# Optimization experiments

Measured on AMD Instinct MI355X. Metric: run time of the kernel, lower is better.

## Reference

```python
import jax, jax.numpy as jnp
import numpy as np
import math

DIM = 512
HEADS = 8
DHEAD = DIM // HEADS            # 64
NB_FEATURES = int(DHEAD * math.log(DHEAD))  # 266
B, N = 2, 2048
CHUNK = 128                     # chunk size for the causal scan
EPS = 1e-4


def gaussian_orthogonal_random_matrix(nb_rows, nb_cols, rng):
    # blocks of orthogonal rows (Q^T of QR of a gaussian), scaled by chi-distributed norms
    blocks = []
    n_full = nb_rows // nb_cols
    for _ in range(n_full):
        q, _ = np.linalg.qr(rng.standard_normal((nb_cols, nb_cols)))
        blocks.append(q.T)
    rem = nb_rows - n_full * nb_cols
    if rem > 0:
        q, _ = np.linalg.qr(rng.standard_normal((nb_cols, nb_cols)))
        blocks.append(q.T[:rem])
    mat = np.concatenate(blocks, axis=0)
    multiplier = np.linalg.norm(rng.standard_normal((nb_rows, nb_cols)), axis=1)
    return (multiplier[:, None] * mat).astype(np.float32)


def setup_inputs() -> dict:
    key = jax.random.key(0)
    k1, k2, k3 = jax.random.split(key, 3)
    rng = np.random.default_rng(0)
    x = jax.random.normal(k1, (B, N, DIM), dtype=jnp.float32)
    w_qkv = jax.random.normal(k2, (DIM, 3 * DIM), dtype=jnp.float32) / math.sqrt(DIM)
    w_out = jax.random.normal(k3, (DIM, DIM), dtype=jnp.float32) / math.sqrt(DIM)
    b_out = jnp.zeros((DIM,), dtype=jnp.float32)
    proj = jnp.asarray(gaussian_orthogonal_random_matrix(NB_FEATURES, DHEAD, rng))
    return {"x": x, "w_qkv": w_qkv, "w_out": w_out, "b_out": b_out, "proj": proj}


def softmax_kernel(data, proj, is_query):
    # data: [b,h,n,d], proj: [m,d]
    d = data.shape[-1]
    data_normalizer = d ** -0.25
    ratio = proj.shape[0] ** -0.5
    data_dash = jnp.einsum('bhnd,md->bhnm', data_normalizer * data, proj)
    diag_data = jnp.sum(data * data, axis=-1, keepdims=True) * 0.5 * (data_normalizer ** 2)
    if is_query:
        stab = jnp.max(data_dash, axis=-1, keepdims=True)
    else:
        stab = jnp.max(data_dash)
    return ratio * (jnp.exp(data_dash - diag_data - stab) + EPS)


def causal_linear_attention(q, k, v, chunk=CHUNK):
    # q,k: [b,h,n,m]; v: [b,h,n,d]
    # out_n = sum_m q_nm * (sum_{i<=n} k_im v_i) / (sum_{i<=n} k_im)   (per-feature normalization,
    # identical to causal_linear_attention_noncuda), computed in chunks for memory efficiency.
    b, h, n, m = q.shape
    d = v.shape[-1]
    nc = n // chunk
    qc = jnp.moveaxis(q.reshape(b, h, nc, chunk, m), 2, 0)  # [nc,b,h,C,m]
    kc = jnp.moveaxis(k.reshape(b, h, nc, chunk, m), 2, 0)
    vc = jnp.moveaxis(v.reshape(b, h, nc, chunk, d), 2, 0)

    def step(carry, inp):
        kv_state, ksum_state = carry            # [b,h,m,d], [b,h,m]
        qch, kch, vch = inp                     # [b,h,C,m], [b,h,C,m], [b,h,C,d]
        ksum = ksum_state[:, :, None, :] + jnp.cumsum(kch, axis=2)          # [b,h,C,m]
        ctx = kv_state[:, :, None, :, :] + jnp.cumsum(
            jnp.einsum('bhcm,bhcd->bhcmd', kch, vch), axis=2)               # [b,h,C,m,d]
        out = jnp.einsum('bhcm,bhcmd->bhcd', qch, ctx / ksum[..., None])
        return (ctx[:, :, -1], ksum[:, :, -1]), out

    init = (jnp.zeros((b, h, m, d), q.dtype), jnp.zeros((b, h, m), q.dtype))
    _, outs = jax.lax.scan(step, init, (qc, kc, vc))
    return jnp.moveaxis(outs, 0, 2).reshape(b, h, n, d)


def reference(x, w_qkv, w_out, b_out, proj):
    b, n, _ = x.shape
    qkv = x @ w_qkv                                   # [b,n,3*dim]
    q, k, v = jnp.split(qkv, 3, axis=-1)
    split = lambda t: t.reshape(b, n, HEADS, DHEAD).transpose(0, 2, 1, 3)  # b h n d
    q, k, v = split(q), split(k), split(v)
    qp = softmax_kernel(q, proj, is_query=True)       # [b,h,n,m]
    kp = softmax_kernel(k, proj, is_query=False)
    out = causal_linear_attention(qp, kp, v)          # [b,h,n,d]
    out = out.transpose(0, 2, 1, 3).reshape(b, n, DIM)
    return out @ w_out + b_out
```

## Files before the change

kernel.cpp:

```cpp
#include <hip/hip_runtime.h>
#include <math.h>

#define DIMX 512
#define NHEADS 8
#define DH 64
#define MF 266
#define MP 272
#define MPS 288
#define NB 2
#define NSEQ 2048
#define NROWS (NB*NSEQ)
#define NBH 16
#define CHK 64
#define NCH 32
#define EPSF 1e-4f
#define LDT 40
#define LDP 72

typedef __attribute__((ext_vector_type(8))) short short8;
typedef __attribute__((ext_vector_type(4))) float f32x4;
typedef unsigned short ushort_t;

__device__ __forceinline__ unsigned fkey(float f){
    unsigned u = __float_as_uint(f);
    return (f < 0.0f) ? ~u : (u | 0x80000000u);
}
__device__ __forceinline__ float fdec(unsigned k){
    unsigned u = (k & 0x80000000u) ? (k & 0x7fffffffu) : ~k;
    return __uint_as_float(u);
}
__device__ __forceinline__ float b2f(ushort_t u){
    return __uint_as_float(((unsigned)u) << 16);
}

__device__ __forceinline__ void bsplit(float a, ushort_t& h, ushort_t& l){
    unsigned u = __float_as_uint(a);
    unsigned r = (u + 0x7fffu + ((u >> 16) & 1u)) & 0xffff0000u;
    h = (ushort_t)(r >> 16);
    float res = a - __uint_as_float(r);
    unsigned v = __float_as_uint(res);
    unsigned r2 = v + 0x7fffu + ((v >> 16) & 1u);
    l = (ushort_t)(r2 >> 16);
}

__global__ __launch_bounds__(256) void split_kernel(
    const float* __restrict__ A, ushort_t* __restrict__ H, ushort_t* __restrict__ L, int total4)
{
    int i = blockIdx.x * 256 + threadIdx.x;
    if (i >= total4) return;
    float4 f = ((const float4*)A)[i];
    ushort_t h0,h1,h2,h3,l0,l1,l2,l3;
    bsplit(f.x,h0,l0); bsplit(f.y,h1,l1); bsplit(f.z,h2,l2); bsplit(f.w,h3,l3);
    ((ushort4*)H)[i] = make_ushort4(h0,h1,h2,h3);
    ((ushort4*)L)[i] = make_ushort4(l0,l1,l2,l3);
}

__global__ __launch_bounds__(256) void splitT_kernel(
    const float* __restrict__ W, ushort_t* __restrict__ Th, ushort_t* __restrict__ Tl,
    int K, int N)
{
    __shared__ ushort_t Sh[64][72], Sl[64][72];
    const int k0 = blockIdx.y * 64, n0 = blockIdx.x * 64;
    const int tid = threadIdx.x;
    {
        const int kk = tid >> 4, nq = (tid & 15) * 4;
        for (int p = 0; p < 4; p++) {
            int k = p*16 + kk;
            float4 f = *(const float4*)&W[(size_t)(k0 + k)*N + n0 + nq];
            ushort_t h, l;
            bsplit(f.x,h,l); Sh[nq+0][k]=h; Sl[nq+0][k]=l;
            bsplit(f.y,h,l); Sh[nq+1][k]=h; Sl[nq+1][k]=l;
            bsplit(f.z,h,l); Sh[nq+2][k]=h; Sl[nq+2][k]=l;
            bsplit(f.w,h,l); Sh[nq+3][k]=h; Sl[nq+3][k]=l;
        }
    }
    __syncthreads();
    {
        const int n = tid >> 2, ks = (tid & 3) * 16;
        for (int q = 0; q < 2; q++) {
            uint4 vh = *(const uint4*)&Sh[n][ks + q*8];
            uint4 vl = *(const uint4*)&Sl[n][ks + q*8];
            *(uint4*)&Th[(size_t)(n0 + n)*K + k0 + ks + q*8] = vh;
            *(uint4*)&Tl[(size_t)(n0 + n)*K + k0 + ks + q*8] = vl;
        }
    }
}

__global__ __launch_bounds__(256) void splitP_kernel(
    const float* __restrict__ proj, ushort_t* __restrict__ ph, ushort_t* __restrict__ pl,
    unsigned* __restrict__ gmax, float nrm)
{
    int idx = blockIdx.x * 256 + threadIdx.x;
    if (idx == 0) *gmax = 0u;
    if (idx >= MPS*64/4) return;
    int m = idx >> 4, kq = (idx & 15) * 4;
    ushort4 h4 = make_ushort4(0,0,0,0), l4 = make_ushort4(0,0,0,0);
    if (m < MF) {
        float4 f = *(const float4*)&proj[m*64 + kq];
        ushort_t hh[4], ll[4];
        bsplit(f.x*nrm,hh[0],ll[0]); bsplit(f.y*nrm,hh[1],ll[1]);
        bsplit(f.z*nrm,hh[2],ll[2]); bsplit(f.w*nrm,hh[3],ll[3]);
        h4 = make_ushort4(hh[0],hh[1],hh[2],hh[3]);
        l4 = make_ushort4(ll[0],ll[1],ll[2],ll[3]);
    }
    *(ushort4*)&ph[(size_t)m*64 + kq] = h4;
    *(ushort4*)&pl[(size_t)m*64 + kq] = l4;
}

__global__ __launch_bounds__(256) void gemm_bf16s(
    const ushort_t* __restrict__ Ah, const ushort_t* __restrict__ Al,
    const ushort_t* __restrict__ Bh, const ushort_t* __restrict__ Bl,
    const float* __restrict__ bias, float* __restrict__ C,
    int M, int N, int K)
{
    __shared__ ushort_t sAh[128*LDT], sAl[128*LDT], sBh[128*LDT], sBl[128*LDT];
    const int tid = threadIdx.x;
    const int m0 = blockIdx.y * 128, n0 = blockIdx.x * 128;
    const int lane = tid & 63, w = tid >> 6;
    const int wr = w >> 1, wc = w & 1;
    const int lr = lane & 15;
    const int lsu = (lane >> 4) * 8;
    const int r = tid >> 1, sg = (tid & 1) * 16;
    const size_t gA = (size_t)(m0 + r)*K + sg;
    const size_t gB = (size_t)(n0 + r)*K + sg;

    f32x4 acc[4][4];
    #pragma unroll
    for (int i=0;i<4;i++)
        #pragma unroll
        for (int j=0;j<4;j++) acc[i][j] = (f32x4){0.f,0.f,0.f,0.f};

    for (int k0 = 0; k0 < K; k0 += 32) {
        uint4 a0 = *(const uint4*)&Ah[gA + k0];
        uint4 a1 = *(const uint4*)&Ah[gA + k0 + 8];
        uint4 a2 = *(const uint4*)&Al[gA + k0];
        uint4 a3 = *(const uint4*)&Al[gA + k0 + 8];
        uint4 b0 = *(const uint4*)&Bh[gB + k0];
        uint4 b1 = *(const uint4*)&Bh[gB + k0 + 8];
        uint4 b2 = *(const uint4*)&Bl[gB + k0];
        uint4 b3 = *(const uint4*)&Bl[gB + k0 + 8];
        __syncthreads();
        *(uint4*)&sAh[r*LDT + sg]     = a0;
        *(uint4*)&sAh[r*LDT + sg + 8] = a1;
        *(uint4*)&sAl[r*LDT + sg]     = a2;
        *(uint4*)&sAl[r*LDT + sg + 8] = a3;
        *(uint4*)&sBh[r*LDT + sg]     = b0;
        *(uint4*)&sBh[r*LDT + sg + 8] = b1;
        *(uint4*)&sBl[r*LDT + sg]     = b2;
        *(uint4*)&sBl[r*LDT + sg + 8] = b3;
        __syncthreads();
        short8 afh[4], afl[4], bfh[4], bfl[4];
        #pragma unroll
        for (int f = 0; f < 4; f++) {
            int ra = (wr*64 + f*16 + lr)*LDT + lsu;
            int rb = (wc*64 + f*16 + lr)*LDT + lsu;
            afh[f] = *(const short8*)&sAh[ra];
            afl[f] = *(const short8*)&sAl[ra];
            bfh[f] = *(const short8*)&sBh[rb];
            bfl[f] = *(const short8*)&sBl[rb];
        }
        #pragma unroll
        for (int i = 0; i < 4; i++)
            #pragma unroll
            for (int j = 0; j < 4; j++) {
                acc[i][j] = __builtin_amdgcn_mfma_f32_16x16x32_bf16(afh[i], bfh[j], acc[i][j], 0, 0, 0);
                acc[i][j] = __builtin_amdgcn_mfma_f32_16x16x32_bf16(afh[i], bfl[j], acc[i][j], 0, 0, 0);
                acc[i][j] = __builtin_amdgcn_mfma_f32_16x16x32_bf16(afl[i], bfh[j], acc[i][j], 0, 0, 0);
            }
    }
    const int crow = (lane >> 4) * 4, ccol = lane & 15;
    #pragma unroll
    for (int i = 0; i < 4; i++) {
        #pragma unroll
        for (int j = 0; j < 4; j++) {
            int col = n0 + wc*64 + j*16 + ccol;
            float bb = bias ? bias[col] : 0.f;
            #pragma unroll
            for (int rr = 0; rr < 4; rr++) {
                int row = m0 + wr*64 + i*16 + crow + rr;
                C[(size_t)row*N + col] = acc[i][j][rr] + bb;
            }
        }
    }
}

__global__ __launch_bounds__(256) void feat_mfma5(
    const float* __restrict__ qkv,
    const ushort_t* __restrict__ pjh, const ushort_t* __restrict__ pjl,
    ushort_t* __restrict__ qph, ushort_t* __restrict__ qpl,
    ushort_t* __restrict__ kph, ushort_t* __restrict__ kpl,
    float* __restrict__ diagq, float* __restrict__ diagk,
    unsigned* __restrict__ rowmax, unsigned* __restrict__ gmax)
{
    const int tid = threadIdx.x;
    const bool isq = (blockIdx.z == 0);
    const int coff = isq ? 0 : DIMX;
    ushort_t* __restrict__ oh = isq ? qph : kph;
    ushort_t* __restrict__ ol = isq ? qpl : kpl;
    float* __restrict__ dgo = isq ? diagq : diagk;
    const int bh = blockIdx.y, b = bh >> 3, h = bh & 7;
    const int mhalf = blockIdx.x & 1;
    const int n0 = (blockIdx.x >> 1) * 64;
    const int lane = tid & 63, w = tid >> 6;
    const int cn = lane & 15, g = lane >> 4;

    short8 bDh[2], bDl[2];
    float dg;
    {
        const int row = w*16 + cn;
        const float* src = &qkv[(size_t)(b*NSEQ + n0 + row)*(3*DIMX) + coff + h*DH];
        float4 u0 = *(const float4*)&src[g*8];
        float4 u1 = *(const float4*)&src[g*8 + 4];
        float4 u2 = *(const float4*)&src[32 + g*8];
        float4 u3 = *(const float4*)&src[32 + g*8 + 4];
        float v0[8] = {u0.x,u0.y,u0.z,u0.w,u1.x,u1.y,u1.z,u1.w};
        float v1[8] = {u2.x,u2.y,u2.z,u2.w,u3.x,u3.y,u3.z,u3.w};
        float ss = 0.f;
        #pragma unroll
        for (int p = 0; p < 8; p++) ss = fmaf(v0[p],v0[p], fmaf(v1[p],v1[p], ss));
        ss += __shfl_xor(ss, 16, 64);
        ss += __shfl_xor(ss, 32, 64);
        dg = 0.0625f * ss;
        #pragma unroll
        for (int p = 0; p < 8; p++) {
            ushort_t hh2, ll2;
            bsplit(v0[p], hh2, ll2); bDh[0][p] = (short)hh2; bDl[0][p] = (short)ll2;
            bsplit(v1[p], hh2, ll2); bDh[1][p] = (short)hh2; bDl[1][p] = (short)ll2;
        }
    }
    const size_t rowidx = (size_t)bh*NSEQ + n0 + w*16 + cn;
    if (mhalf == 0 && g == 0) dgo[rowidx] = dg;

    const int mbase = mhalf * 9;
    f32x4 acc[9];
    #pragma unroll
    for (int t = 0; t < 9; t++) acc[t] = (f32x4){0.f,0.f,0.f,0.f};
    #pragma unroll
    for (int t = 0; t < 9; ++t) {
        const size_t rb = (size_t)((mbase + t)*16 + cn)*64 + g*8;
        short8 a0h = *(const short8*)&pjh[rb];
        short8 a1h = *(const short8*)&pjh[rb + 32];
        short8 a0l = *(const short8*)&pjl[rb];
        short8 a1l = *(const short8*)&pjl[rb + 32];
        acc[t] = __builtin_amdgcn_mfma_f32_16x16x32_bf16(a0h, bDh[0], acc[t], 0, 0, 0);
        acc[t] = __builtin_amdgcn_mfma_f32_16x16x32_bf16(a0h, bDl[0], acc[t], 0, 0, 0);
        acc[t] = __builtin_amdgcn_mfma_f32_16x16x32_bf16(a0l, bDh[0], acc[t], 0, 0, 0);
        acc[t] = __builtin_amdgcn_mfma_f32_16x16x32_bf16(a1h, bDh[1], acc[t], 0, 0, 0);
        acc[t] = __builtin_amdgcn_mfma_f32_16x16x32_bf16(a1h, bDl[1], acc[t], 0, 0, 0);
        acc[t] = __builtin_amdgcn_mfma_f32_16x16x32_bf16(a1l, bDh[1], acc[t], 0, 0, 0);
    }
    const size_t orow = rowidx * MPS;
    const int mb0 = g*4;
    float mx = -1e30f;
    #pragma unroll
    for (int t = 0; t < 9; ++t) {
        ushort_t hh[4], ll[4];
        #pragma unroll
        for (int rr = 0; rr < 4; rr++) {
            int m = (mbase + t)*16 + mb0 + rr;
            float v = (m < MF) ? acc[t][rr] : 0.f;
            if (m < MF) mx = fmaxf(mx, v);
            bsplit(v, hh[rr], ll[rr]);
        }
        *(ushort4*)&oh[orow + (mbase + t)*16 + mb0] = make_ushort4(hh[0],hh[1],hh[2],hh[3]);
        *(ushort4*)&ol[orow + (mbase + t)*16 + mb0] = make_ushort4(ll[0],ll[1],ll[2],ll[3]);
    }
    if (isq) {
        mx = fmaxf(mx, __shfl_xor(mx, 16, 64));
        mx = fmaxf(mx, __shfl_xor(mx, 32, 64));
        if (g == 0) atomicMax(&rowmax[rowidx], fkey(mx));
    } else {
        #pragma unroll
        for (int o = 1; o < 64; o <<= 1) mx = fmaxf(mx, __shfl_xor(mx, o, 64));
        if (lane == 0) atomicMax(gmax, fkey(mx));
    }
}

__global__ __launch_bounds__(256) void qkexp_kernel(
    ushort_t* __restrict__ qph, ushort_t* __restrict__ qpl,
    ushort_t* __restrict__ kph, ushort_t* __restrict__ kpl,
    const float* __restrict__ diagq, const float* __restrict__ diagk,
    const unsigned* __restrict__ rowmax, const unsigned* __restrict__ gmax, float ratio)
{
    unsigned gid = blockIdx.x * 256u + threadIdx.x;
    if (gid >= (unsigned)(NBH*NSEQ*(MPS/4))) return;
    const bool isq = (blockIdx.y == 0);
    unsigned row = gid / (MPS/4);
    int mq = (int)(gid % (MPS/4)) * 4;
    const float sub = isq ? (diagq[row] + fdec(rowmax[row]))
                          : (diagk[row] + fdec(*gmax));
    ushort_t* __restrict__ ph = isq ? qph : kph;
    ushort_t* __restrict__ pl = isq ? qpl : kpl;
    size_t idx = (size_t)row*MPS + mq;
    ushort4 h4 = *(const ushort4*)&ph[idx];
    ushort4 l4 = *(const ushort4*)&pl[idx];
    float dv[4] = {b2f(h4.x)+b2f(l4.x), b2f(h4.y)+b2f(l4.y),
                   b2f(h4.z)+b2f(l4.z), b2f(h4.w)+b2f(l4.w)};
    ushort_t hh[4], ll[4];
    #pragma unroll
    for (int j = 0; j < 4; j++) {
        float kv = (mq + j < MF) ? ratio * (expf(dv[j] - sub) + EPSF) : 0.f;
        bsplit(kv, hh[j], ll[j]);
    }
    *(ushort4*)&ph[idx] = make_ushort4(hh[0],hh[1],hh[2],hh[3]);
    *(ushort4*)&pl[idx] = make_ushort4(ll[0],ll[1],ll[2],ll[3]);
}

__global__ __launch_bounds__(320) void chunk_sums_kernel(
    const ushort_t* __restrict__ kph, const ushort_t* __restrict__ kpl,
    const float* __restrict__ qkv,
    float* __restrict__ ckvT, float* __restrict__ cksum)
{
    __shared__ float vs[CHK][DH];
    const int tid = threadIdx.x;
    const int c = blockIdx.x, bh = blockIdx.y, b = bh >> 3, h = bh & 7;
    for (int idx = tid; idx < CHK*16; idx += 320) {
        int i = idx >> 4, q = idx & 15;
        *(float4*)&vs[i][q*4] =
            *(const float4*)&qkv[(size_t)(b*NSEQ + c*CHK + i)*(3*DIMX) + 2*DIMX + h*DH + q*4];
    }
    __syncthreads();
    if (tid >= 272) return;
    const int mg = tid % 68, dg = tid / 68;
    float acc[4][16] = {};
    float ks[4] = {0.f,0.f,0.f,0.f};
    const size_t kbase = (size_t)(bh*NSEQ + c*CHK)*MPS + mg*4;
    for (int i = 0; i < CHK; i++) {
        ushort4 kh = *(const ushort4*)&kph[kbase + (size_t)i*MPS];
        ushort4 kl = *(const ushort4*)&kpl[kbase + (size_t)i*MPS];
        float kr[4] = {b2f(kh.x)+b2f(kl.x), b2f(kh.y)+b2f(kl.y),
                       b2f(kh.z)+b2f(kl.z), b2f(kh.w)+b2f(kl.w)};
        if (dg == 0) { ks[0]+=kr[0]; ks[1]+=kr[1]; ks[2]+=kr[2]; ks[3]+=kr[3]; }
        #pragma unroll
        for (int t = 0; t < 4; t++) {
            float4 vv = *(const float4*)&vs[i][dg*16 + t*4];
            float vr[4] = {vv.x,vv.y,vv.z,vv.w};
            #pragma unroll
            for (int mi=0;mi<4;mi++){
                acc[mi][t*4+0] = fmaf(kr[mi], vr[0], acc[mi][t*4+0]);
                acc[mi][t*4+1] = fmaf(kr[mi], vr[1], acc[mi][t*4+1]);
                acc[mi][t*4+2] = fmaf(kr[mi], vr[2], acc[mi][t*4+2]);
                acc[mi][t*4+3] = fmaf(kr[mi], vr[3], acc[mi][t*4+3]);
            }
        }
    }
    const size_t tbase = (size_t)(bh*NCH + c)*64;
    #pragma unroll
    for (int dd = 0; dd < 16; dd++) {
        int d = dg*16 + dd;
        *(float4*)&ckvT[(tbase + d)*MP + mg*4] =
            make_float4(acc[0][dd], acc[1][dd], acc[2][dd], acc[3][dd]);
    }
    if (dg == 0) {
        #pragma unroll
        for (int mi=0;mi<4;mi++)
            cksum[(size_t)(bh*NCH + c)*MP + mg*4 + mi] = ks[mi];
    }
}

__global__ __launch_bounds__(256) void prefix_ckvT_kernel(
    const float* __restrict__ ckvT, ushort_t* __restrict__ cth, ushort_t* __restrict__ ctl)
{
    const int bh = blockIdx.y;
    const int dm = blockIdx.x * 256 + threadIdx.x;
    if (dm >= 64*MPS) return;
    const int d = dm / MPS, m = dm % MPS;
    if (m < MP) {
        float run = 0.f;
        #pragma unroll
        for (int c = 0; c < NCH; c++) {
            size_t row = (size_t)(bh*NCH + c)*64 + d;
            ushort_t h, l;
            bsplit(run, h, l);
            cth[row*MPS + m] = h; ctl[row*MPS + m] = l;
            run += ckvT[row*MP + m];
        }
    } else {
        #pragma unroll
        for (int c = 0; c < NCH; c++) {
            size_t row = (size_t)(bh*NCH + c)*64 + d;
            cth[row*MPS + m] = 0; ctl[row*MPS + m] = 0;
        }
    }
}

__global__ __launch_bounds__(320) void prefix_ksum_kernel(float* __restrict__ cksum)
{
    const int bh = blockIdx.x;
    const int m = threadIdx.x;
    if (m >= MP) return;
    float run = 0.f;
    #pragma unroll
    for (int c = 0; c < NCH; c++) {
        size_t idx = (size_t)(bh*NCH + c)*MP + m;
        float v = cksum[idx];
        cksum[idx] = run;
        run += v;
    }
}

__global__ __launch_bounds__(320) void qprime_kernel(
    ushort_t* __restrict__ qph, ushort_t* __restrict__ qpl,
    const ushort_t* __restrict__ kph, const ushort_t* __restrict__ kpl,
    const float* __restrict__ cksum)
{
    const int c = blockIdx.x, bh = blockIdx.y;
    const int m = threadIdx.x;
    if (m >= MPS) return;
    size_t base = (size_t)(bh*NSEQ + c*CHK)*MPS + m;
    if (m < MF) {
        float run = cksum[(size_t)(bh*NCH + c)*MP + m];
        for (int i = 0; i < CHK; i++) {
            size_t idx = base + (size_t)i*MPS;
            run += b2f(kph[idx]) + b2f(kpl[idx]);
            float q = b2f(qph[idx]) + b2f(qpl[idx]);
            q /= run;
            ushort_t h, l;
            bsplit(q, h, l);
            qph[idx] = h; qpl[idx] = l;
        }
    } else {
        for (int i = 0; i < CHK; i++) {
            size_t idx = base + (size_t)i*MPS;
            qph[idx] = 0; qpl[idx] = 0;
        }
    }
}

__global__ __launch_bounds__(256) void attn_mfma(
    const ushort_t* __restrict__ qph, const ushort_t* __restrict__ qpl,
    const ushort_t* __restrict__ kph, const ushort_t* __restrict__ kpl,
    const ushort_t* __restrict__ cth, const ushort_t* __restrict__ ctl,
    const float* __restrict__ qkv,
    ushort_t* __restrict__ aout_h, ushort_t* __restrict__ aout_l)
{
    __shared__ ushort_t tQh[64*LDT], tQl[64*LDT];
    __shared__ ushort_t tKh[64*LDT], tKl[64*LDT];
    __shared__ ushort_t tSh[64*LDT], tSl[64*LDT];
    __shared__ ushort_t VTh[64*LDP], VTl[64*LDP];
    __shared__ ushort_t Ph[64*LDP],  Pl[64*LDP];
    const int tid = threadIdx.x;
    const int c = blockIdx.x, bh = blockIdx.y, b = bh >> 3, hh = bh & 7;
    const size_t rowg = (size_t)bh*NSEQ + c*CHK;
    const size_t rowx = (size_t)b*NSEQ + c*CHK;
    const size_t sbase = (size_t)(bh*NCH + c)*64;

    {
        const int j = tid >> 2, dq = (tid & 3) * 16;
        const float* vsrc = &qkv[(rowx + j)*(3*DIMX) + 2*DIMX + hh*DH + dq];
        #pragma unroll
        for (int p = 0; p < 4; p++) {
            float4 f = *(const float4*)&vsrc[p*4];
            float vr[4] = {f.x,f.y,f.z,f.w};
            #pragma unroll
            for (int wv = 0; wv < 4; wv++) {
                ushort_t h, l;
                bsplit(vr[wv], h, l);
                VTh[(dq + p*4 + wv)*LDP + j] = h;
                VTl[(dq + p*4 + wv)*LDP + j] = l;
            }
        }
    }

    const int lane = tid & 63, w = tid >> 6;
    const int wr = w >> 1, wc = w & 1;
    const int fr = lane & 15, fk = (lane >> 4) * 8;
    const int srow = tid >> 2, sseg = (tid & 3) * 8;
    f32x4 accP[2][2], accO[2][2];
    #pragma unroll
    for (int i=0;i<2;i++)
        #pragma unroll
        for (int j=0;j<2;j++){ accP[i][j]=(f32x4){0,0,0,0}; accO[i][j]=(f32x4){0,0,0,0}; }

    for (int m0 = 0; m0 < MPS; m0 += 32) {
        uint4 gq_h = *(const uint4*)&qph[(rowg + srow)*MPS + m0 + sseg];
        uint4 gq_l = *(const uint4*)&qpl[(rowg + srow)*MPS + m0 + sseg];
        uint4 gk_h = *(const uint4*)&kph[(rowg + srow)*MPS + m0 + sseg];
        uint4 gk_l = *(const uint4*)&kpl[(rowg + srow)*MPS + m0 + sseg];
        uint4 gs_h = *(const uint4*)&cth[(sbase + srow)*MPS + m0 + sseg];
        uint4 gs_l = *(const uint4*)&ctl[(sbase + srow)*MPS + m0 + sseg];
        __syncthreads();
        *(uint4*)&tQh[srow*LDT + sseg] = gq_h;
        *(uint4*)&tQl[srow*LDT + sseg] = gq_l;
        *(uint4*)&tKh[srow*LDT + sseg] = gk_h;
        *(uint4*)&tKl[srow*LDT + sseg] = gk_l;
        *(uint4*)&tSh[srow*LDT + sseg] = gs_h;
        *(uint4*)&tSl[srow*LDT + sseg] = gs_l;
        __syncthreads();
        short8 aQh[2], aQl[2], bKh[2], bKl[2], bSh[2], bSl[2];
        #pragma unroll
        for (int f = 0; f < 2; f++) {
            int ra = (wr*32 + f*16 + fr)*LDT + fk;
            int rb = (wc*32 + f*16 + fr)*LDT + fk;
            aQh[f] = *(const short8*)&tQh[ra];
            aQl[f] = *(const short8*)&tQl[ra];
            bKh[f] = *(const short8*)&tKh[rb];
            bKl[f] = *(const short8*)&tKl[rb];
            bSh[f] = *(const short8*)&tSh[rb];
            bSl[f] = *(const short8*)&tSl[rb];
        }
        #pragma unroll
        for (int i = 0; i < 2; i++)
            #pragma unroll
            for (int j = 0; j < 2; j++) {
                accP[i][j] = __builtin_amdgcn_mfma_f32_16x16x32_bf16(aQh[i], bKh[j], accP[i][j], 0, 0, 0);
                accP[i][j] = __builtin_amdgcn_mfma_f32_16x16x32_bf16(aQh[i], bKl[j], accP[i][j], 0, 0, 0);
                accP[i][j] = __builtin_amdgcn_mfma_f32_16x16x32_bf16(aQl[i], bKh[j], accP[i][j], 0, 0, 0);
                accO[i][j] = __builtin_amdgcn_mfma_f32_16x16x32_bf16(aQh[i], bSh[j], accO[i][j], 0, 0, 0);
                accO[i][j] = __builtin_amdgcn_mfma_f32_16x16x32_bf16(aQh[i], bSl[j], accO[i][j], 0, 0, 0);
                accO[i][j] = __builtin_amdgcn_mfma_f32_16x16x32_bf16(aQl[i], bSh[j], accO[i][j], 0, 0, 0);
            }
    }

    __syncthreads();
    {
        const int crow = (lane >> 4) * 4, ccol = lane & 15;
        #pragma unroll
        for (int i = 0; i < 2; i++)
            #pragma unroll
            for (int j = 0; j < 2; j++) {
                int colg = wc*32 + j*16 + ccol;
                #pragma unroll
                for (int rr = 0; rr < 4; rr++) {
                    int rowg2 = wr*32 + i*16 + crow + rr;
                    float v = (colg <= rowg2) ? accP[i][j][rr] : 0.f;
                    ushort_t h, l;
                    bsplit(v, h, l);
                    Ph[rowg2*LDP + colg] = h;
                    Pl[rowg2*LDP + colg] = l;
                }
            }
    }
    __syncthreads();

    #pragma unroll
    for (int js = 0; js < 2; js++) {
        short8 aPh[2], aPl[2], bVh[2], bVl[2];
        #pragma unroll
        for (int f = 0; f < 2; f++) {
            int ra = (wr*32 + f*16 + fr)*LDP + js*32 + fk;
            int rb = (wc*32 + f*16 + fr)*LDP + js*32 + fk;
            aPh[f] = *(const short8*)&Ph[ra];
            aPl[f] = *(const short8*)&Pl[ra];
            bVh[f] = *(const short8*)&VTh[rb];
            bVl[f] = *(const short8*)&VTl[rb];
        }
        #pragma unroll
        for (int i = 0; i < 2; i++)
            #pragma unroll
            for (int j = 0; j < 2; j++) {
                accO[i][j] = __builtin_amdgcn_mfma_f32_16x16x32_bf16(aPh[i], bVh[j], accO[i][j], 0, 0, 0);
                accO[i][j] = __builtin_amdgcn_mfma_f32_16x16x32_bf16(aPh[i], bVl[j], accO[i][j], 0, 0, 0);
                accO[i][j] = __builtin_amdgcn_mfma_f32_16x16x32_bf16(aPl[i], bVh[j], accO[i][j], 0, 0, 0);
            }
    }

    __syncthreads();
    {
        const int crow = (lane >> 4) * 4, ccol = lane & 15;
        #pragma unroll
        for (int i = 0; i < 2; i++)
            #pragma unroll
            for (int j = 0; j < 2; j++) {
                int d = wc*32 + j*16 + ccol;
                #pragma unroll
                for (int rr = 0; rr < 4; rr++) {
                    int row = wr*32 + i*16 + crow + rr;
                    ushort_t h, l;
                    bsplit(accO[i][j][rr], h, l);
                    Ph[row*LDP + d] = h;
                    Pl[row*LDP + d] = l;
                }
            }
    }
    __syncthreads();
    #pragma unroll
    for (int p = 0; p < 2; p++) {
        int u = tid + p*256;
        int row = u >> 3, c8 = u & 7;
        size_t o = (rowx + row)*DIMX + hh*DH + c8*8;
        *(uint4*)&aout_h[o] = *(const uint4*)&Ph[row*LDP + c8*8];
        *(uint4*)&aout_l[o] = *(const uint4*)&Pl[row*LDP + c8*8];
    }
}

extern "C" void kernel_launch(void* const* d_in, const int* in_sizes, int n_in,
                              void* d_out, int out_size, void* d_ws, size_t ws_size,
                              hipStream_t stream)
{
    (void)in_sizes; (void)n_in; (void)out_size; (void)ws_size;
    const float* x     = (const float*)d_in[0];
    const float* w_qkv = (const float*)d_in[1];
    const float* w_out = (const float*)d_in[2];
    const float* b_out = (const float*)d_in[3];
    const float* proj  = (const float*)d_in[4];
    float* out = (float*)d_out;

    char* ws = (char*)d_ws;
    size_t off = 0;
    auto alloc = [&](size_t bytes) -> char* {
        char* p = ws + off;
        off += (bytes + 255) & ~(size_t)255;
        return p;
    };
    float* qkv       = (float*)alloc((size_t)NROWS*3*DIMX*sizeof(float));
    float* ckvT      = (float*)alloc((size_t)NBH*NCH*64*MP*sizeof(float));
    ushort_t* qph    = (ushort_t*)alloc((size_t)NBH*NSEQ*MPS*sizeof(ushort_t));
    ushort_t* qpl    = (ushort_t*)alloc((size_t)NBH*NSEQ*MPS*sizeof(ushort_t));
    ushort_t* kph    = (ushort_t*)alloc((size_t)NBH*NSEQ*MPS*sizeof(ushort_t));
    ushort_t* kpl    = (ushort_t*)alloc((size_t)NBH*NSEQ*MPS*sizeof(ushort_t));
    ushort_t* cth    = (ushort_t*)alloc((size_t)NBH*NCH*64*MPS*sizeof(ushort_t));
    ushort_t* ctl    = (ushort_t*)alloc((size_t)NBH*NCH*64*MPS*sizeof(ushort_t));
    float* cksum     = (float*)alloc((size_t)NBH*NCH*MP*sizeof(float));
    float* diagq     = (float*)alloc((size_t)NBH*NSEQ*sizeof(float));
    float* diagk     = (float*)alloc((size_t)NBH*NSEQ*sizeof(float));
    unsigned* rowmax = (unsigned*)alloc((size_t)NBH*NSEQ*sizeof(unsigned));
    unsigned* gmax   = (unsigned*)alloc(256);
    ushort_t* xs_h   = (ushort_t*)alloc((size_t)NROWS*DIMX*sizeof(ushort_t));
    ushort_t* xs_l   = (ushort_t*)alloc((size_t)NROWS*DIMX*sizeof(ushort_t));
    ushort_t* wqt_h  = (ushort_t*)alloc((size_t)(3*DIMX)*DIMX*sizeof(ushort_t));
    ushort_t* wqt_l  = (ushort_t*)alloc((size_t)(3*DIMX)*DIMX*sizeof(ushort_t));
    ushort_t* wot_h  = (ushort_t*)alloc((size_t)DIMX*DIMX*sizeof(ushort_t));
    ushort_t* wot_l  = (ushort_t*)alloc((size_t)DIMX*DIMX*sizeof(ushort_t));
    ushort_t* pjh    = (ushort_t*)alloc((size_t)MPS*64*sizeof(ushort_t));
    ushort_t* pjl    = (ushort_t*)alloc((size_t)MPS*64*sizeof(ushort_t));
    ushort_t* aout_h = xs_h;
    ushort_t* aout_l = xs_l;

    const float nrm   = (float)pow(64.0, -0.25);
    const float ratio = (float)(1.0 / sqrt(266.0));

    hipMemsetAsync(rowmax, 0, (size_t)NBH*NSEQ*sizeof(unsigned), stream);
    split_kernel<<<dim3((NROWS*DIMX/4 + 255)/256), 256, 0, stream>>>(x, xs_h, xs_l, NROWS*DIMX/4);
    splitT_kernel<<<dim3(3*DIMX/64, DIMX/64), 256, 0, stream>>>(w_qkv, wqt_h, wqt_l, DIMX, 3*DIMX);
    splitT_kernel<<<dim3(DIMX/64, DIMX/64), 256, 0, stream>>>(w_out, wot_h, wot_l, DIMX, DIMX);
    splitP_kernel<<<dim3((MPS*64/4 + 255)/256), 256, 0, stream>>>(proj, pjh, pjl, gmax, nrm);
    gemm_bf16s<<<dim3(3*DIMX/128, NROWS/128), 256, 0, stream>>>(
        xs_h, xs_l, wqt_h, wqt_l, nullptr, qkv, NROWS, 3*DIMX, DIMX);
    feat_mfma5<<<dim3(64, 16, 2), 256, 0, stream>>>(
        qkv, pjh, pjl, qph, qpl, kph, kpl, diagq, diagk, rowmax, gmax);
    qkexp_kernel<<<dim3((NBH*NSEQ*(MPS/4) + 255)/256, 2), 256, 0, stream>>>(
        qph, qpl, kph, kpl, diagq, diagk, rowmax, gmax, ratio);
    chunk_sums_kernel<<<dim3(NCH, NBH), 320, 0, stream>>>(kph, kpl, qkv, ckvT, cksum);
    prefix_ckvT_kernel<<<dim3((64*MPS + 255)/256, NBH), 256, 0, stream>>>(ckvT, cth, ctl);
    prefix_ksum_kernel<<<dim3(NBH), 320, 0, stream>>>(cksum);
    qprime_kernel<<<dim3(NCH, NBH), 320, 0, stream>>>(qph, qpl, kph, kpl, cksum);
    attn_mfma<<<dim3(NCH, NBH), 256, 0, stream>>>(
        qph, qpl, kph, kpl, cth, ctl, qkv, aout_h, aout_l);
    gemm_bf16s<<<dim3(DIMX/128, NROWS/128), 256, 0, stream>>>(
        aout_h, aout_l, wot_h, wot_l, b_out, out, NROWS, DIMX, DIMX);
}
```

Measured before the change: 294.0 us.

## Fuse exp normalization into chunk sums and qprime, drop qkexp pass

```diff
diff --git a/kernel.cpp b/kernel.cpp
--- a/kernel.cpp
+++ b/kernel.cpp
@@ -184,23 +184,21 @@
     }
 }
 
-__global__ __launch_bounds__(256) void feat_mfma5(
+__global__ __launch_bounds__(256) void feat_mfma6(
     const float* __restrict__ qkv,
     const ushort_t* __restrict__ pjh, const ushort_t* __restrict__ pjl,
     ushort_t* __restrict__ qph, ushort_t* __restrict__ qpl,
     ushort_t* __restrict__ kph, ushort_t* __restrict__ kpl,
     float* __restrict__ diagq, float* __restrict__ diagk,
-    unsigned* __restrict__ rowmax, unsigned* __restrict__ gmax)
+    float* __restrict__ rowmax, unsigned* __restrict__ gmax)
 {
     const int tid = threadIdx.x;
     const bool isq = (blockIdx.z == 0);
     const int coff = isq ? 0 : DIMX;
     ushort_t* __restrict__ oh = isq ? qph : kph;
     ushort_t* __restrict__ ol = isq ? qpl : kpl;
-    float* __restrict__ dgo = isq ? diagq : diagk;
     const int bh = blockIdx.y, b = bh >> 3, h = bh & 7;
-    const int mhalf = blockIdx.x & 1;
-    const int n0 = (blockIdx.x >> 1) * 64;
+    const int n0 = blockIdx.x * 64;
     const int lane = tid & 63, w = tid >> 6;
     const int cn = lane & 15, g = lane >> 4;
 
@@ -229,46 +227,41 @@
         }
     }
     const size_t rowidx = (size_t)bh*NSEQ + n0 + w*16 + cn;
-    if (mhalf == 0 && g == 0) dgo[rowidx] = dg;
-
-    const int mbase = mhalf * 9;
-    f32x4 acc[9];
-    #pragma unroll
-    for (int t = 0; t < 9; t++) acc[t] = (f32x4){0.f,0.f,0.f,0.f};
-    #pragma unroll
-    for (int t = 0; t < 9; ++t) {
-        const size_t rb = (size_t)((mbase + t)*16 + cn)*64 + g*8;
+    if (g == 0) { (isq ? diagq : diagk)[rowidx] = dg; }
+
+    const size_t orow = rowidx * MPS;
+    const int mb0 = g*4;
+    float mx = -1e30f;
+
+    #pragma unroll 2
+    for (int mt = 0; mt < 18; ++mt) {
+        const size_t rb = (size_t)(mt*16 + cn)*64 + g*8;
         short8 a0h = *(const short8*)&pjh[rb];
         short8 a1h = *(const short8*)&pjh[rb + 32];
         short8 a0l = *(const short8*)&pjl[rb];
         short8 a1l = *(const short8*)&pjl[rb + 32];
-        acc[t] = __builtin_amdgcn_mfma_f32_16x16x32_bf16(a0h, bDh[0], acc[t], 0, 0, 0);
-        acc[t] = __builtin_amdgcn_mfma_f32_16x16x32_bf16(a0h, bDl[0], acc[t], 0, 0, 0);
-        acc[t] = __builtin_amdgcn_mfma_f32_16x16x32_bf16(a0l, bDh[0], acc[t], 0, 0, 0);
-        acc[t] = __builtin_amdgcn_mfma_f32_16x16x32_bf16(a1h, bDh[1], acc[t], 0, 0, 0);
-        acc[t] = __builtin_amdgcn_mfma_f32_16x16x32_bf16(a1h, bDl[1], acc[t], 0, 0, 0);
-        acc[t] = __builtin_amdgcn_mfma_f32_16x16x32_bf16(a1l, bDh[1], acc[t], 0, 0, 0);
-    }
-    const size_t orow = rowidx * MPS;
-    const int mb0 = g*4;
-    float mx = -1e30f;
-    #pragma unroll
-    for (int t = 0; t < 9; ++t) {
+        f32x4 acc = (f32x4){0.f,0.f,0.f,0.f};
+        acc = __builtin_amdgcn_mfma_f32_16x16x32_bf16(a0h, bDh[0], acc, 0, 0, 0);
+        acc = __builtin_amdgcn_mfma_f32_16x16x32_bf16(a0h, bDl[0], acc, 0, 0, 0);
+        acc = __builtin_amdgcn_mfma_f32_16x16x32_bf16(a0l, bDh[0], acc, 0, 0, 0);
+        acc = __builtin_amdgcn_mfma_f32_16x16x32_bf16(a1h, bDh[1], acc, 0, 0, 0);
+        acc = __builtin_amdgcn_mfma_f32_16x16x32_bf16(a1h, bDl[1], acc, 0, 0, 0);
+        acc = __builtin_amdgcn_mfma_f32_16x16x32_bf16(a1l, bDh[1], acc, 0, 0, 0);
         ushort_t hh[4], ll[4];
         #pragma unroll
         for (int rr = 0; rr < 4; rr++) {
-            int m = (mbase + t)*16 + mb0 + rr;
-            float v = (m < MF) ? acc[t][rr] : 0.f;
+            int m = mt*16 + mb0 + rr;
+            float v = (m < MF) ? acc[rr] : 0.f;
             if (m < MF) mx = fmaxf(mx, v);
             bsplit(v, hh[rr], ll[rr]);
         }
-        *(ushort4*)&oh[orow + (mbase + t)*16 + mb0] = make_ushort4(hh[0],hh[1],hh[2],hh[3]);
-        *(ushort4*)&ol[orow + (mbase + t)*16 + mb0] = make_ushort4(ll[0],ll[1],ll[2],ll[3]);
+        *(ushort4*)&oh[orow + mt*16 + mb0] = make_ushort4(hh[0],hh[1],hh[2],hh[3]);
+        *(ushort4*)&ol[orow + mt*16 + mb0] = make_ushort4(ll[0],ll[1],ll[2],ll[3]);
     }
     if (isq) {
         mx = fmaxf(mx, __shfl_xor(mx, 16, 64));
         mx = fmaxf(mx, __shfl_xor(mx, 32, 64));
-        if (g == 0) atomicMax(&rowmax[rowidx], fkey(mx));
+        if (g == 0) rowmax[rowidx] = mx;
     } else {
         #pragma unroll
         for (int o = 1; o < 64; o <<= 1) mx = fmaxf(mx, __shfl_xor(mx, o, 64));
@@ -276,40 +269,11 @@
     }
 }
 
-__global__ __launch_bounds__(256) void qkexp_kernel(
-    ushort_t* __restrict__ qph, ushort_t* __restrict__ qpl,
-    ushort_t* __restrict__ kph, ushort_t* __restrict__ kpl,
-    const float* __restrict__ diagq, const float* __restrict__ diagk,
-    const unsigned* __restrict__ rowmax, const unsigned* __restrict__ gmax, float ratio)
-{
-    unsigned gid = blockIdx.x * 256u + threadIdx.x;
-    if (gid >= (unsigned)(NBH*NSEQ*(MPS/4))) return;
-    const bool isq = (blockIdx.y == 0);
-    unsigned row = gid / (MPS/4);
-    int mq = (int)(gid % (MPS/4)) * 4;
-    const float sub = isq ? (diagq[row] + fdec(rowmax[row]))
-                          : (diagk[row] + fdec(*gmax));
-    ushort_t* __restrict__ ph = isq ? qph : kph;
-    ushort_t* __restrict__ pl = isq ? qpl : kpl;
-    size_t idx = (size_t)row*MPS + mq;
-    ushort4 h4 = *(const ushort4*)&ph[idx];
-    ushort4 l4 = *(const ushort4*)&pl[idx];
-    float dv[4] = {b2f(h4.x)+b2f(l4.x), b2f(h4.y)+b2f(l4.y),
-                   b2f(h4.z)+b2f(l4.z), b2f(h4.w)+b2f(l4.w)};
-    ushort_t hh[4], ll[4];
-    #pragma unroll
-    for (int j = 0; j < 4; j++) {
-        float kv = (mq + j < MF) ? ratio * (expf(dv[j] - sub) + EPSF) : 0.f;
-        bsplit(kv, hh[j], ll[j]);
-    }
-    *(ushort4*)&ph[idx] = make_ushort4(hh[0],hh[1],hh[2],hh[3]);
-    *(ushort4*)&pl[idx] = make_ushort4(ll[0],ll[1],ll[2],ll[3]);
-}
-
 __global__ __launch_bounds__(320) void chunk_sums_kernel(
     const ushort_t* __restrict__ kph, const ushort_t* __restrict__ kpl,
-    const float* __restrict__ qkv,
-    float* __restrict__ ckvT, float* __restrict__ cksum)
+    const float* __restrict__ qkv, const float* __restrict__ diagk,
+    const unsigned* __restrict__ gmax,
+    float* __restrict__ ckvT, float* __restrict__ cksum, float ratio)
 {
     __shared__ float vs[CHK][DH];
     const int tid = threadIdx.x;
@@ -321,15 +285,26 @@
     }
     __syncthreads();
     if (tid >= 272) return;
+    const float stab = fdec(*gmax);
     const int mg = tid % 68, dg = tid / 68;
     float acc[4][16] = {};
     float ks[4] = {0.f,0.f,0.f,0.f};
-    const size_t kbase = (size_t)(bh*NSEQ + c*CHK)*MPS + mg*4;
+    const size_t rb0 = (size_t)bh*NSEQ + c*CHK;
+    const size_t kbase = rb0*MPS + mg*4;
     for (int i = 0; i < CHK; i++) {
+        const float sub = diagk[rb0 + i] + stab;
         ushort4 kh = *(const ushort4*)&kph[kbase + (size_t)i*MPS];
         ushort4 kl = *(const ushort4*)&kpl[kbase + (size_t)i*MPS];
-        float kr[4] = {b2f(kh.x)+b2f(kl.x), b2f(kh.y)+b2f(kl.y),
+        float dr[4] = {b2f(kh.x)+b2f(kl.x), b2f(kh.y)+b2f(kl.y),
                        b2f(kh.z)+b2f(kl.z), b2f(kh.w)+b2f(kl.w)};
+        float kr[4];
+        #pragma unroll
+        for (int mi = 0; mi < 4; mi++) {
+            float kv = (mg*4 + mi < MF) ? ratio * (expf(dr[mi] - sub) + EPSF) : 0.f;
+            ushort_t whh, wll;
+            bsplit(kv, whh, wll);
+            kr[mi] = b2f(whh) + b2f(wll);
+        }
         if (dg == 0) { ks[0]+=kr[0]; ks[1]+=kr[1]; ks[2]+=kr[2]; ks[3]+=kr[3]; }
         #pragma unroll
         for (int t = 0; t < 4; t++) {
@@ -401,19 +376,30 @@
 
 __global__ __launch_bounds__(320) void qprime_kernel(
     ushort_t* __restrict__ qph, ushort_t* __restrict__ qpl,
-    const ushort_t* __restrict__ kph, const ushort_t* __restrict__ kpl,
-    const float* __restrict__ cksum)
+    ushort_t* __restrict__ kph, ushort_t* __restrict__ kpl,
+    const float* __restrict__ cksum, const float* __restrict__ diagq,
+    const float* __restrict__ diagk, const float* __restrict__ rowmax,
+    const unsigned* __restrict__ gmax, float ratio)
 {
     const int c = blockIdx.x, bh = blockIdx.y;
     const int m = threadIdx.x;
     if (m >= MPS) return;
-    size_t base = (size_t)(bh*NSEQ + c*CHK)*MPS + m;
+    const size_t rb0 = (size_t)bh*NSEQ + c*CHK;
+    size_t base = rb0*MPS + m;
     if (m < MF) {
+        const float stab = fdec(*gmax);
         float run = cksum[(size_t)(bh*NCH + c)*MP + m];
         for (int i = 0; i < CHK; i++) {
             size_t idx = base + (size_t)i*MPS;
-            run += b2f(kph[idx]) + b2f(kpl[idx]);
-            float q = b2f(qph[idx]) + b2f(qpl[idx]);
+            float kraw = b2f(kph[idx]) + b2f(kpl[idx]);
+            float kv = ratio * (expf(kraw - diagk[rb0 + i] - stab) + EPSF);
+            ushort_t kh2, kl2;
+            bsplit(kv, kh2, kl2);
+            kph[idx] = kh2; kpl[idx] = kl2;
+            run += b2f(kh2) + b2f(kl2);
+            float sub = diagq[rb0 + i] + rowmax[rb0 + i];
+            float qraw = b2f(qph[idx]) + b2f(qpl[idx]);
+            float q = ratio * (expf(qraw - sub) + EPSF);
             q /= run;
             ushort_t h, l;
             bsplit(q, h, l);
@@ -423,6 +409,7 @@
         for (int i = 0; i < CHK; i++) {
             size_t idx = base + (size_t)i*MPS;
             qph[idx] = 0; qpl[idx] = 0;
+            kph[idx] = 0; kpl[idx] = 0;
         }
     }
 }
@@ -614,7 +601,7 @@
     float* cksum     = (float*)alloc((size_t)NBH*NCH*MP*sizeof(float));
     float* diagq     = (float*)alloc((size_t)NBH*NSEQ*sizeof(float));
     float* diagk     = (float*)alloc((size_t)NBH*NSEQ*sizeof(float));
-    unsigned* rowmax = (unsigned*)alloc((size_t)NBH*NSEQ*sizeof(unsigned));
+    float* rowmax    = (float*)alloc((size_t)NBH*NSEQ*sizeof(float));
     unsigned* gmax   = (unsigned*)alloc(256);
     ushort_t* xs_h   = (ushort_t*)alloc((size_t)NROWS*DIMX*sizeof(ushort_t));
     ushort_t* xs_l   = (ushort_t*)alloc((size_t)NROWS*DIMX*sizeof(ushort_t));
@@ -630,21 +617,20 @@
     const float nrm   = (float)pow(64.0, -0.25);
     const float ratio = (float)(1.0 / sqrt(266.0));
 
-    hipMemsetAsync(rowmax, 0, (size_t)NBH*NSEQ*sizeof(unsigned), stream);
     split_kernel<<<dim3((NROWS*DIMX/4 + 255)/256), 256, 0, stream>>>(x, xs_h, xs_l, NROWS*DIMX/4);
     splitT_kernel<<<dim3(3*DIMX/64, DIMX/64), 256, 0, stream>>>(w_qkv, wqt_h, wqt_l, DIMX, 3*DIMX);
     splitT_kernel<<<dim3(DIMX/64, DIMX/64), 256, 0, stream>>>(w_out, wot_h, wot_l, DIMX, DIMX);
     splitP_kernel<<<dim3((MPS*64/4 + 255)/256), 256, 0, stream>>>(proj, pjh, pjl, gmax, nrm);
     gemm_bf16s<<<dim3(3*DIMX/128, NROWS/128), 256, 0, stream>>>(
         xs_h, xs_l, wqt_h, wqt_l, nullptr, qkv, NROWS, 3*DIMX, DIMX);
-    feat_mfma5<<<dim3(64, 16, 2), 256, 0, stream>>>(
+    feat_mfma6<<<dim3(32, 16, 2), 256, 0, stream>>>(
         qkv, pjh, pjl, qph, qpl, kph, kpl, diagq, diagk, rowmax, gmax);
-    qkexp_kernel<<<dim3((NBH*NSEQ*(MPS/4) + 255)/256, 2), 256, 0, stream>>>(
-        qph, qpl, kph, kpl, diagq, diagk, rowmax, gmax, ratio);
-    chunk_sums_kernel<<<dim3(NCH, NBH), 320, 0, stream>>>(kph, kpl, qkv, ckvT, cksum);
+    chunk_sums_kernel<<<dim3(NCH, NBH), 320, 0, stream>>>(
+        kph, kpl, qkv, diagk, gmax, ckvT, cksum, ratio);
     prefix_ckvT_kernel<<<dim3((64*MPS + 255)/256, NBH), 256, 0, stream>>>(ckvT, cth, ctl);
     prefix_ksum_kernel<<<dim3(NBH), 320, 0, stream>>>(cksum);
-    qprime_kernel<<<dim3(NCH, NBH), 320, 0, stream>>>(qph, qpl, kph, kpl, cksum);
+    qprime_kernel<<<dim3(NCH, NBH), 320, 0, stream>>>(
+        qph, qpl, kph, kpl, cksum, diagq, diagk, rowmax, gmax, ratio);
     attn_mfma<<<dim3(NCH, NBH), 256, 0, stream>>>(
         qph, qpl, kph, kpl, cth, ctl, qkv, aout_h, aout_l);
     gemm_bf16s<<<dim3(DIMX/128, NROWS/128), 256, 0, stream>>>(
```

Result: no change. 290.4 us (-1.2%).
